# Optimization experiments

Hardware: AMD Instinct MI355X
Metric: run time of the kernel (lower is better)

## Reference

```python
import jax, jax.numpy as jnp
import numpy as np

M, P, B = 64, 256, 4096  # blocks per row/col, block size, batch


def setup_inputs() -> dict:
    key = jax.random.key(0)
    ks = jax.random.split(key, 6)
    u = lambda k, shape: jax.random.uniform(k, shape, jnp.float32, -0.1, 0.1)
    return {
        "x": jax.random.normal(ks[0], (B, M * P), dtype=jnp.float32),
        "Wd": u(ks[1], (M, P, P)),      # diag blocks (nn.Linear weights)
        "Wu": u(ks[2], (M - 1, P, P)),  # upper off-diagonal blocks
        "Wl": u(ks[3], (M - 1, P, P)),  # lower off-diagonal blocks
        "Wtr": u(ks[4], (P, P)),        # top-right corner block (periodic)
        "Wbl": u(ks[5], (P, P)),        # bottom-left corner block (periodic)
    }


def reference(x, Wd, Wu, Wl, Wtr, Wbl):
    # BlockXDiag forward, diag_type='tri', periodic=True, transpose=False,
    # bias=False, activation=None (identity). nn.Linear: o = x @ W.T
    Bsz = x.shape[0]
    xb = x.reshape(Bsz, M, P)  # [B, M, P]
    # diagonal: result[:, i] = x_i @ Wd[i].T  -> batched over all M blocks
    out = jnp.einsum('bip,iqp->biq', xb, Wd)
    # upper band: result[:, i] += x_{i+1} @ Wu[i].T, i in [0, M-2]
    out = out.at[:, : M - 1].add(jnp.einsum('bip,iqp->biq', xb[:, 1:], Wu))
    # lower band: result[:, i] += x_{i-1} @ Wl[i-1].T, i in [1, M-1]
    out = out.at[:, 1:].add(jnp.einsum('bip,iqp->biq', xb[:, : M - 1], Wl))
    # periodic corners
    out = out.at[:, 0].add(xb[:, M - 1] @ Wtr.T)
    out = out.at[:, M - 1].add(xb[:, 0] @ Wbl.T)
    return out.reshape(Bsz, M * P)
```

## Files before the change

### kernel.cpp

```cpp
#include <hip/hip_runtime.h>


#define MB   64
#define PB   256
#define NPR  16384
#define BM   128
#define BN   128
#define BK   32
#define KTOT 768

typedef __bf16 bf16x8 __attribute__((ext_vector_type(8)));
typedef float  f32x4  __attribute__((ext_vector_type(4)));
typedef unsigned short u16x4 __attribute__((ext_vector_type(4)));

__device__ __forceinline__ unsigned short f2bf(float f) {
    unsigned u = __float_as_uint(f);
    u += 0x7fffu + ((u >> 16) & 1u);
    return (unsigned short)(u >> 16);
}

__global__ __launch_bounds__(256, 2)
void bxd_kernel(const float* __restrict__ x,
                const float* __restrict__ Wd,
                const float* __restrict__ Wu,
                const float* __restrict__ Wl,
                const float* __restrict__ Wtr,
                const float* __restrict__ Wbl,
                float* __restrict__ out)
{
    __shared__ unsigned short sA[BM * BK];
    __shared__ unsigned short sB[BN * BK];

    const int i  = blockIdx.x >> 1;
    const int nt = blockIdx.x & 1;
    const int mt = blockIdx.y;

    const int t    = threadIdx.x;
    const int lane = t & 63;
    const int wave = t >> 6;
    const int wm   = wave & 1;
    const int wn   = wave >> 1;
    const int quad = lane >> 4;
    const int l16  = lane & 15;

    const int srow = t >> 3;
    const int scol = (t & 7) * 4;

    const float* wptr[3];
    wptr[0] = (i == 0)      ? Wtr : (Wl + (size_t)(i - 1) * (PB * PB));
    wptr[1] = Wd + (size_t)i * (PB * PB);
    wptr[2] = (i == MB - 1) ? Wbl : (Wu + (size_t)i * (PB * PB));
    const int jblk[3] = { (i + MB - 1) & (MB - 1), i, (i + 1) & (MB - 1) };

    f32x4 acc[4][4];
    #pragma unroll
    for (int a = 0; a < 4; ++a)
        #pragma unroll
        for (int b = 0; b < 4; ++b)
            acc[a][b] = (f32x4){0.f, 0.f, 0.f, 0.f};

    for (int kt = 0; kt < KTOT / BK; ++kt) {
        const int c  = kt >> 3;
        const int kb = kt & 7;

        const float* aSrc = x + (size_t)(mt * BM + srow) * NPR
                              + jblk[c] * PB + kb * BK + scol;
        const float* bSrc = wptr[c] + (size_t)(nt * BN + srow) * PB
                              + kb * BK + scol;

        float4 av[4], bv[4];
        #pragma unroll
        for (int p = 0; p < 4; ++p) {
            av[p] = *(const float4*)(aSrc + (size_t)p * 32 * NPR);
            bv[p] = *(const float4*)(bSrc + (size_t)p * 32 * PB);
        }

        __syncthreads();
        #pragma unroll
        for (int p = 0; p < 4; ++p) {
            u16x4 ra = { f2bf(av[p].x), f2bf(av[p].y), f2bf(av[p].z), f2bf(av[p].w) };
            *(u16x4*)&sA[(srow + p * 32) * BK + scol] = ra;
            u16x4 rb = { f2bf(bv[p].x), f2bf(bv[p].y), f2bf(bv[p].z), f2bf(bv[p].w) };
            *(u16x4*)&sB[(srow + p * 32) * BK + scol] = rb;
        }
        __syncthreads();

        bf16x8 afrag[4], bfrag[4];
        #pragma unroll
        for (int mi = 0; mi < 4; ++mi)
            afrag[mi] = *(const bf16x8*)&sA[(wm * 64 + mi * 16 + l16) * BK + quad * 8];
        #pragma unroll
        for (int ni = 0; ni < 4; ++ni)
            bfrag[ni] = *(const bf16x8*)&sB[(wn * 64 + ni * 16 + l16) * BK + quad * 8];

        #pragma unroll
        for (int mi = 0; mi < 4; ++mi)
            #pragma unroll
            for (int ni = 0; ni < 4; ++ni)
                acc[mi][ni] = __builtin_amdgcn_mfma_f32_16x16x32_bf16(
                    afrag[mi], bfrag[ni], acc[mi][ni], 0, 0, 0);
    }

    const int colb = i * PB + nt * BN + wn * 64;
    #pragma unroll
    for (int mi = 0; mi < 4; ++mi) {
        #pragma unroll
        for (int ni = 0; ni < 4; ++ni) {
            #pragma unroll
            for (int r = 0; r < 4; ++r) {
                const int row = mt * BM + wm * 64 + mi * 16 + quad * 4 + r;
                out[(size_t)row * NPR + colb + ni * 16 + l16] = acc[mi][ni][r];
            }
        }
    }
}

extern "C" void kernel_launch(void* const* d_in, const int* in_sizes, int n_in,
                              void* d_out, int out_size, void* d_ws, size_t ws_size,
                              hipStream_t stream) {
    const float* x   = (const float*)d_in[0];
    const float* Wd  = (const float*)d_in[1];
    const float* Wu  = (const float*)d_in[2];
    const float* Wl  = (const float*)d_in[3];
    const float* Wtr = (const float*)d_in[4];
    const float* Wbl = (const float*)d_in[5];
    float* out = (float*)d_out;

    dim3 grid(MB * 2, 4096 / BM, 1);
    dim3 block(256, 1, 1);
    hipLaunchKernelGGL(bxd_kernel, grid, block, 0, stream,
                       x, Wd, Wu, Wl, Wtr, Wbl, out);
}
```

Measured before the change: 768.8 us.

## Prefetch next K-tile into registers, pad LDS rows, raise occupancy bound

The global loads for the next K-tile are now issued right after the LDS store barrier, so they overlap with the LDS fragment reads and MFMA work of the current tile instead of stalling at the top of each iteration. LDS rows are padded from 32 to 40 bf16 elements to reduce bank conflicts on the 16-byte fragment reads. The launch bound is raised to 3 blocks per SM. The extra prefetch registers (32 floats) combined with the tighter register budget could cause spills.

```diff
diff --git a/kernel.cpp b/kernel.cpp
--- a/kernel.cpp
+++ b/kernel.cpp
@@ -7,7 +7,9 @@
 #define BM   128
 #define BN   128
 #define BK   32
+#define BKP  40
 #define KTOT 768
+#define NKT  (KTOT / BK)
 
 typedef __bf16 bf16x8 __attribute__((ext_vector_type(8)));
 typedef float  f32x4  __attribute__((ext_vector_type(4)));
@@ -19,7 +21,7 @@
     return (unsigned short)(u >> 16);
 }
 
-__global__ __launch_bounds__(256, 2)
+__global__ __launch_bounds__(256, 3)
 void bxd_kernel(const float* __restrict__ x,
                 const float* __restrict__ Wd,
                 const float* __restrict__ Wu,
@@ -28,8 +30,8 @@
                 const float* __restrict__ Wbl,
                 float* __restrict__ out)
 {
-    __shared__ unsigned short sA[BM * BK];
-    __shared__ unsigned short sB[BN * BK];
+    __shared__ unsigned short sA[BM * BKP];
+    __shared__ unsigned short sB[BN * BKP];
 
     const int i  = blockIdx.x >> 1;
     const int nt = blockIdx.x & 1;
@@ -46,11 +48,28 @@
     const int srow = t >> 3;
     const int scol = (t & 7) * 4;
 
-    const float* wptr[3];
-    wptr[0] = (i == 0)      ? Wtr : (Wl + (size_t)(i - 1) * (PB * PB));
-    wptr[1] = Wd + (size_t)i * (PB * PB);
-    wptr[2] = (i == MB - 1) ? Wbl : (Wu + (size_t)i * (PB * PB));
-    const int jblk[3] = { (i + MB - 1) & (MB - 1), i, (i + 1) & (MB - 1) };
+    const float* bB0 = ((i == 0)      ? Wtr : (Wl + (size_t)(i - 1) * (PB * PB)))
+                       + (size_t)(nt * BN + srow) * PB + scol;
+    const float* bB1 = (Wd + (size_t)i * (PB * PB))
+                       + (size_t)(nt * BN + srow) * PB + scol;
+    const float* bB2 = ((i == MB - 1) ? Wbl : (Wu + (size_t)i * (PB * PB)))
+                       + (size_t)(nt * BN + srow) * PB + scol;
+    const int jprev = (i + MB - 1) & (MB - 1);
+    const int jnext = (i + 1) & (MB - 1);
+    const float* aBase = x + (size_t)(mt * BM + srow) * NPR + scol;
+
+    auto issue = [&](int kt, float4 av[4], float4 bv[4]) {
+        const int c  = kt >> 3;
+        const int kb = kt & 7;
+        const int jb = (c == 0) ? jprev : (c == 1) ? i : jnext;
+        const float* aS = aBase + jb * PB + kb * BK;
+        const float* bS = ((c == 0) ? bB0 : (c == 1) ? bB1 : bB2) + kb * BK;
+        #pragma unroll
+        for (int p = 0; p < 4; ++p) {
+            av[p] = *(const float4*)(aS + (size_t)p * 32 * NPR);
+            bv[p] = *(const float4*)(bS + (size_t)p * 32 * PB);
+        }
+    };
 
     f32x4 acc[4][4];
     #pragma unroll
@@ -59,39 +78,30 @@
         for (int b = 0; b < 4; ++b)
             acc[a][b] = (f32x4){0.f, 0.f, 0.f, 0.f};
 
-    for (int kt = 0; kt < KTOT / BK; ++kt) {
-        const int c  = kt >> 3;
-        const int kb = kt & 7;
+    float4 av[4], bv[4];
+    issue(0, av, bv);
 
-        const float* aSrc = x + (size_t)(mt * BM + srow) * NPR
-                              + jblk[c] * PB + kb * BK + scol;
-        const float* bSrc = wptr[c] + (size_t)(nt * BN + srow) * PB
-                              + kb * BK + scol;
-
-        float4 av[4], bv[4];
-        #pragma unroll
-        for (int p = 0; p < 4; ++p) {
-            av[p] = *(const float4*)(aSrc + (size_t)p * 32 * NPR);
-            bv[p] = *(const float4*)(bSrc + (size_t)p * 32 * PB);
-        }
-
+    for (int kt = 0; kt < NKT; ++kt) {
         __syncthreads();
         #pragma unroll
         for (int p = 0; p < 4; ++p) {
             u16x4 ra = { f2bf(av[p].x), f2bf(av[p].y), f2bf(av[p].z), f2bf(av[p].w) };
-            *(u16x4*)&sA[(srow + p * 32) * BK + scol] = ra;
+            *(u16x4*)&sA[(srow + p * 32) * BKP + scol] = ra;
             u16x4 rb = { f2bf(bv[p].x), f2bf(bv[p].y), f2bf(bv[p].z), f2bf(bv[p].w) };
-            *(u16x4*)&sB[(srow + p * 32) * BK + scol] = rb;
+            *(u16x4*)&sB[(srow + p * 32) * BKP + scol] = rb;
         }
         __syncthreads();
+
+        float4 an[4], bn[4];
+        if (kt < NKT - 1) issue(kt + 1, an, bn);
 
         bf16x8 afrag[4], bfrag[4];
         #pragma unroll
         for (int mi = 0; mi < 4; ++mi)
-            afrag[mi] = *(const bf16x8*)&sA[(wm * 64 + mi * 16 + l16) * BK + quad * 8];
+            afrag[mi] = *(const bf16x8*)&sA[(wm * 64 + mi * 16 + l16) * BKP + quad * 8];
         #pragma unroll
         for (int ni = 0; ni < 4; ++ni)
-            bfrag[ni] = *(const bf16x8*)&sB[(wn * 64 + ni * 16 + l16) * BK + quad * 8];
+            bfrag[ni] = *(const bf16x8*)&sB[(wn * 64 + ni * 16 + l16) * BKP + quad * 8];
 
         #pragma unroll
         for (int mi = 0; mi < 4; ++mi)
@@ -99,6 +109,11 @@
             for (int ni = 0; ni < 4; ++ni)
                 acc[mi][ni] = __builtin_amdgcn_mfma_f32_16x16x32_bf16(
                     afrag[mi], bfrag[ni], acc[mi][ni], 0, 0, 0);
+
+        if (kt < NKT - 1) {
+            #pragma unroll
+            for (int p = 0; p < 4; ++p) { av[p] = an[p]; bv[p] = bn[p]; }
+        }
     }
 
     const int colb = i * PB + nt * BN + wn * 64;
```

Measured after the change: 803.1 us. 1.04x slower.
